# Kernel optimization log

Measured on AMD Instinct MI355X. Metric: run time of the kernel, lower is better.

## Reference

```python
import jax, jax.numpy as jnp
import numpy as np

N = 1024
IN_CH = 128
EDGE_CH = 32
OUT_CH = 128


def setup_inputs() -> dict:
    key = jax.random.key(0)
    ks = jax.random.split(key, 8)
    return {
        "node_mat": jax.random.normal(ks[0], (N, IN_CH), dtype=jnp.float32),
        "adj": jax.random.uniform(ks[1], (N, N), dtype=jnp.float32),
        "edge_adj": jax.random.uniform(ks[2], (EDGE_CH, N, N), dtype=jnp.float32),
        "node_weight": jax.random.normal(ks[3], (IN_CH, OUT_CH), dtype=jnp.float32) * 0.05,
        "edge_lay_1": jax.random.normal(ks[4], (EDGE_CH, OUT_CH - 1), dtype=jnp.float32) * 0.05,
        "edge_lay_2": jax.random.normal(ks[5], (OUT_CH - 1, OUT_CH), dtype=jnp.float32) * 0.05,
        "root": jax.random.normal(ks[6], (IN_CH, OUT_CH), dtype=jnp.float32) * 0.05,
        "bias": jax.random.normal(ks[7], (OUT_CH,), dtype=jnp.float32) * 0.05,
    }


def reference(node_mat, adj, edge_adj, node_weight, edge_lay_1, edge_lay_2, root, bias):
    # node message passing: adj-weighted sum of transformed node features  [N, out]
    sum_filter_node_msgs = adj @ (node_mat @ node_weight)
    # edge MLP: 2-layer with ReLU, applied over the edge-channel axis
    # edge_adj: [E, N, N]; edge_lay_1: [E, out-1] -> h1: [out-1, N, N]
    h1 = jnp.maximum(jnp.einsum('enm,eb->bnm', edge_adj, edge_lay_1), 0.0)
    # h1: [out-1, N, N]; edge_lay_2: [out-1, out] -> h2: [out, N, N]
    h2 = jnp.einsum('bnm,bo->onm', h1, edge_lay_2)
    # adjacency-weighted compression: e_compress[n, o] = sum_m h2[o, n, m] * adj[n, m]
    e_compress = jnp.einsum('onm,nm->no', h2, adj)
    root_info = node_mat @ root
    return sum_filter_node_msgs + e_compress + root_info + bias
```

## Files before the change

### kernel.cpp

```cpp
#include <hip/hip_runtime.h>
#include <hip/hip_bf16.h>

#define NN 1024
#define IN_CH 128
#define EDGE_CH 32
#define OUT_CH 128

typedef __attribute__((ext_vector_type(8))) short bf16x8;
typedef __attribute__((ext_vector_type(4))) float f32x4;

static __device__ __forceinline__ short f2bf(float f) {
    union { float f; unsigned u; } v; v.f = f;
    unsigned r = v.u + 0x7FFFu + ((v.u >> 16) & 1u);
    return (short)(r >> 16);
}

__global__ void node_gemm_kernel(const float* __restrict__ node_mat,
                                 const float* __restrict__ node_weight,
                                 const float* __restrict__ root,
                                 short* __restrict__ PT,
                                 float* __restrict__ R) {
    __shared__ float nm[2 * IN_CH];
    int tid = threadIdx.x;
    int n0 = blockIdx.x * 2;
    nm[tid] = node_mat[n0 * IN_CH + tid];
    __syncthreads();
    int o = tid & 127;
    int h = tid >> 7;
    const float* nr = &nm[h * IN_CH];
    float accp = 0.f, accr = 0.f;
#pragma unroll 8
    for (int c = 0; c < IN_CH; ++c) {
        float x = nr[c];
        accp += x * node_weight[c * OUT_CH + o];
        accr += x * root[c * OUT_CH + o];
    }
    R[(size_t)(n0 + h) * OUT_CH + o] = accr;
    PT[(size_t)o * NN + (n0 + h)] = f2bf(accp);
}

__global__ void edge_out_kernel(const float* __restrict__ edge_adj,
                                const float* __restrict__ adj,
                                const float* __restrict__ L1,
                                const float* __restrict__ L2,
                                const float* __restrict__ R,
                                const float* __restrict__ bias,
                                float* __restrict__ out) {
    int n = blockIdx.x;
    int tid = threadIdx.x;
    int wave = tid >> 6;
    int lane = tid & 63;
    int quad = lane >> 4;
    int col  = lane & 15;

    bf16x8 a_frag[8];
#pragma unroll
    for (int bt = 0; bt < 8; ++bt) {
        int b = bt * 16 + col;
#pragma unroll
        for (int j = 0; j < 8; ++j) {
            int e = quad * 8 + j;
            float v = (b < OUT_CH - 1) ? L1[e * (OUT_CH - 1) + b] : 0.0f;
            a_frag[bt][j] = f2bf(v);
        }
    }

    float g_acc[8][4];
#pragma unroll
    for (int bt = 0; bt < 8; ++bt)
#pragma unroll
        for (int r = 0; r < 4; ++r) g_acc[bt][r] = 0.0f;

    const float* adj_row = adj + (size_t)n * NN;
    const float* ea_base = edge_adj + (size_t)n * NN;

    for (int c = 0; c < 4; ++c) {
        int base = wave * 256 + c * 64;
        float adjv[4];
        bf16x8 bf[4];
#pragma unroll
        for (int s = 0; s < 4; ++s) {
            int m = base + s * 16 + col;
            adjv[s] = adj_row[m];
#pragma unroll
            for (int j = 0; j < 8; ++j) {
                size_t e = (size_t)(quad * 8 + j);
                bf[s][j] = f2bf(ea_base[e * (size_t)(NN * NN) + m]);
            }
        }
#pragma unroll
        for (int s = 0; s < 4; ++s) {
#pragma unroll
            for (int bt = 0; bt < 8; ++bt) {
                f32x4 d = __builtin_amdgcn_mfma_f32_16x16x32_bf16(
                    a_frag[bt], bf[s], (f32x4){0.f, 0.f, 0.f, 0.f}, 0, 0, 0);
#pragma unroll
                for (int r = 0; r < 4; ++r)
                    g_acc[bt][r] += fmaxf(d[r], 0.0f) * adjv[s];
            }
        }
    }

#pragma unroll
    for (int bt = 0; bt < 8; ++bt)
#pragma unroll
        for (int r = 0; r < 4; ++r) {
            float v = g_acc[bt][r];
            v += __shfl_xor(v, 1);
            v += __shfl_xor(v, 2);
            v += __shfl_xor(v, 4);
            v += __shfl_xor(v, 8);
            g_acc[bt][r] = v;
        }

    __shared__ float gred[4][OUT_CH];
    __shared__ float gs[OUT_CH];
    __shared__ float part[2][OUT_CH];
    if (col == 0) {
#pragma unroll
        for (int bt = 0; bt < 8; ++bt)
#pragma unroll
            for (int r = 0; r < 4; ++r)
                gred[wave][bt * 16 + quad * 4 + r] = g_acc[bt][r];
    }
    __syncthreads();
    if (tid < OUT_CH)
        gs[tid] = gred[0][tid] + gred[1][tid] + gred[2][tid] + gred[3][tid];
    __syncthreads();

    int o = tid & 127;
    int hf = tid >> 7;
    float acc = 0.f;
    int blo = hf * 64, bhi = hf ? 127 : 64;
#pragma unroll 8
    for (int b = blo; b < bhi; ++b)
        acc += gs[b] * L2[b * OUT_CH + o];
    part[hf][o] = acc;
    __syncthreads();
    if (tid < 128)
        out[(size_t)n * OUT_CH + tid] =
            part[0][tid] + part[1][tid] + R[(size_t)n * OUT_CH + tid] + bias[tid];
}

__global__ void adjp_kernel(const float* __restrict__ adj,
                            const short* __restrict__ PT,
                            float* __restrict__ out) {
    int blk = blockIdx.x;
    int nb = blk & 63;
    int oh = blk >> 6;
    int tid = threadIdx.x;
    int wave = tid >> 6;
    int lane = tid & 63;
    int quad = lane >> 4;
    int col  = lane & 15;
    int n0 = nb * 16;
    int o0 = oh * 64;

    f32x4 acc[4];
#pragma unroll
    for (int ot = 0; ot < 4; ++ot) acc[ot] = (f32x4){0.f, 0.f, 0.f, 0.f};

    int kbase = wave * 256;
#pragma unroll
    for (int ks = 0; ks < 8; ++ks) {
        int k = kbase + ks * 32 + quad * 8;
        const float* ap = adj + (size_t)(n0 + col) * NN + k;
        f32x4 a0 = *(const f32x4*)ap;
        f32x4 a1 = *(const f32x4*)(ap + 4);
        bf16x8 a;
#pragma unroll
        for (int j = 0; j < 4; ++j) { a[j] = f2bf(a0[j]); a[4 + j] = f2bf(a1[j]); }
#pragma unroll
        for (int ot = 0; ot < 4; ++ot) {
            int o = o0 + ot * 16 + col;
            bf16x8 b = *(const bf16x8*)(PT + (size_t)o * NN + k);
            acc[ot] = __builtin_amdgcn_mfma_f32_16x16x32_bf16(a, b, acc[ot], 0, 0, 0);
        }
    }

    __shared__ float red[4][16][65];
#pragma unroll
    for (int ot = 0; ot < 4; ++ot)
#pragma unroll
        for (int r = 0; r < 4; ++r)
            red[wave][quad * 4 + r][ot * 16 + col] = acc[ot][r];
    __syncthreads();

#pragma unroll
    for (int i = tid; i < 16 * 64; i += 256) {
        int rr = i >> 6;
        int cc = i & 63;
        float v = red[0][rr][cc] + red[1][rr][cc] + red[2][rr][cc] + red[3][rr][cc];
        out[(size_t)(n0 + rr) * OUT_CH + o0 + cc] += v;
    }
}

extern "C" void kernel_launch(void* const* d_in, const int* in_sizes, int n_in,
                              void* d_out, int out_size, void* d_ws, size_t ws_size,
                              hipStream_t stream) {
    const float* node_mat    = (const float*)d_in[0];
    const float* adj         = (const float*)d_in[1];
    const float* edge_adj    = (const float*)d_in[2];
    const float* node_weight = (const float*)d_in[3];
    const float* edge_lay_1  = (const float*)d_in[4];
    const float* edge_lay_2  = (const float*)d_in[5];
    const float* root        = (const float*)d_in[6];
    const float* bias        = (const float*)d_in[7];
    float* out = (float*)d_out;

    short* PT = (short*)d_ws;
    float* R  = (float*)((char*)d_ws + OUT_CH * NN * sizeof(short));

    node_gemm_kernel<<<NN / 2, 256, 0, stream>>>(node_mat, node_weight, root, PT, R);
    edge_out_kernel<<<NN, 256, 0, stream>>>(edge_adj, adj, edge_lay_1, edge_lay_2,
                                            R, bias, out);
    adjp_kernel<<<128, 256, 0, stream>>>(adj, PT, out);
}
```

Baseline: 243.9 us.

## Stage edge_adj through LDS with async global_load_lds double buffering

The edge kernel now loads edge_adj slices directly into a double-buffered LDS tile using global_load_lds 16-byte transfers, instead of scalar strided global loads. Each block rotates its chunk order by block index to spread DRAM access, and the compute for one chunk overlaps the prefetch of the next. Kernel order is swapped so adjp writes R and bias first and the edge kernel accumulates into out, and launch bounds are set for two blocks per CU. The cost is 64KB of LDS per block, which limits occupancy, plus an LDS read-and-convert step before each MFMA.

```diff
diff --git a/kernel.cpp b/kernel.cpp
--- a/kernel.cpp
+++ b/kernel.cpp
@@ -5,6 +5,7 @@
 #define IN_CH 128
 #define EDGE_CH 32
 #define OUT_CH 128
+#define NNSQ ((size_t)NN * (size_t)NN)
 
 typedef __attribute__((ext_vector_type(8))) short bf16x8;
 typedef __attribute__((ext_vector_type(4))) float f32x4;
@@ -39,111 +40,10 @@
     PT[(size_t)o * NN + (n0 + h)] = f2bf(accp);
 }
 
-__global__ void edge_out_kernel(const float* __restrict__ edge_adj,
-                                const float* __restrict__ adj,
-                                const float* __restrict__ L1,
-                                const float* __restrict__ L2,
-                                const float* __restrict__ R,
-                                const float* __restrict__ bias,
-                                float* __restrict__ out) {
-    int n = blockIdx.x;
-    int tid = threadIdx.x;
-    int wave = tid >> 6;
-    int lane = tid & 63;
-    int quad = lane >> 4;
-    int col  = lane & 15;
-
-    bf16x8 a_frag[8];
-#pragma unroll
-    for (int bt = 0; bt < 8; ++bt) {
-        int b = bt * 16 + col;
-#pragma unroll
-        for (int j = 0; j < 8; ++j) {
-            int e = quad * 8 + j;
-            float v = (b < OUT_CH - 1) ? L1[e * (OUT_CH - 1) + b] : 0.0f;
-            a_frag[bt][j] = f2bf(v);
-        }
-    }
-
-    float g_acc[8][4];
-#pragma unroll
-    for (int bt = 0; bt < 8; ++bt)
-#pragma unroll
-        for (int r = 0; r < 4; ++r) g_acc[bt][r] = 0.0f;
-
-    const float* adj_row = adj + (size_t)n * NN;
-    const float* ea_base = edge_adj + (size_t)n * NN;
-
-    for (int c = 0; c < 4; ++c) {
-        int base = wave * 256 + c * 64;
-        float adjv[4];
-        bf16x8 bf[4];
-#pragma unroll
-        for (int s = 0; s < 4; ++s) {
-            int m = base + s * 16 + col;
-            adjv[s] = adj_row[m];
-#pragma unroll
-            for (int j = 0; j < 8; ++j) {
-                size_t e = (size_t)(quad * 8 + j);
-                bf[s][j] = f2bf(ea_base[e * (size_t)(NN * NN) + m]);
-            }
-        }
-#pragma unroll
-        for (int s = 0; s < 4; ++s) {
-#pragma unroll
-            for (int bt = 0; bt < 8; ++bt) {
-                f32x4 d = __builtin_amdgcn_mfma_f32_16x16x32_bf16(
-                    a_frag[bt], bf[s], (f32x4){0.f, 0.f, 0.f, 0.f}, 0, 0, 0);
-#pragma unroll
-                for (int r = 0; r < 4; ++r)
-                    g_acc[bt][r] += fmaxf(d[r], 0.0f) * adjv[s];
-            }
-        }
-    }
-
-#pragma unroll
-    for (int bt = 0; bt < 8; ++bt)
-#pragma unroll
-        for (int r = 0; r < 4; ++r) {
-            float v = g_acc[bt][r];
-            v += __shfl_xor(v, 1);
-            v += __shfl_xor(v, 2);
-            v += __shfl_xor(v, 4);
-            v += __shfl_xor(v, 8);
-            g_acc[bt][r] = v;
-        }
-
-    __shared__ float gred[4][OUT_CH];
-    __shared__ float gs[OUT_CH];
-    __shared__ float part[2][OUT_CH];
-    if (col == 0) {
-#pragma unroll
-        for (int bt = 0; bt < 8; ++bt)
-#pragma unroll
-            for (int r = 0; r < 4; ++r)
-                gred[wave][bt * 16 + quad * 4 + r] = g_acc[bt][r];
-    }
-    __syncthreads();
-    if (tid < OUT_CH)
-        gs[tid] = gred[0][tid] + gred[1][tid] + gred[2][tid] + gred[3][tid];
-    __syncthreads();
-
-    int o = tid & 127;
-    int hf = tid >> 7;
-    float acc = 0.f;
-    int blo = hf * 64, bhi = hf ? 127 : 64;
-#pragma unroll 8
-    for (int b = blo; b < bhi; ++b)
-        acc += gs[b] * L2[b * OUT_CH + o];
-    part[hf][o] = acc;
-    __syncthreads();
-    if (tid < 128)
-        out[(size_t)n * OUT_CH + tid] =
-            part[0][tid] + part[1][tid] + R[(size_t)n * OUT_CH + tid] + bias[tid];
-}
-
 __global__ void adjp_kernel(const float* __restrict__ adj,
                             const short* __restrict__ PT,
+                            const float* __restrict__ R,
+                            const float* __restrict__ bias,
                             float* __restrict__ out) {
     int blk = blockIdx.x;
     int nb = blk & 63;
@@ -191,7 +91,136 @@
         int rr = i >> 6;
         int cc = i & 63;
         float v = red[0][rr][cc] + red[1][rr][cc] + red[2][rr][cc] + red[3][rr][cc];
-        out[(size_t)(n0 + rr) * OUT_CH + o0 + cc] += v;
+        size_t idx = (size_t)(n0 + rr) * OUT_CH + o0 + cc;
+        out[idx] = v + R[idx] + bias[o0 + cc];
+    }
+}
+
+__global__ void __launch_bounds__(256, 2)
+edge_out_kernel(const float* __restrict__ edge_adj,
+                const float* __restrict__ adj,
+                const float* __restrict__ L1,
+                const float* __restrict__ L2,
+                float* __restrict__ out) {
+    int n = blockIdx.x;
+    int tid = threadIdx.x;
+    int wave = tid >> 6;
+    int lane = tid & 63;
+    int quad = lane >> 4;
+    int col  = lane & 15;
+
+    __shared__ __attribute__((aligned(16))) float ea_lds[2][32 * 256];
+
+    bf16x8 a_frag[8];
+#pragma unroll
+    for (int bt = 0; bt < 8; ++bt) {
+        int b = bt * 16 + col;
+#pragma unroll
+        for (int j = 0; j < 8; ++j) {
+            int e = quad * 8 + j;
+            float v = (b < OUT_CH - 1) ? L1[e * (OUT_CH - 1) + b] : 0.0f;
+            a_frag[bt][j] = f2bf(v);
+        }
+    }
+
+    float g_acc[8][4];
+#pragma unroll
+    for (int bt = 0; bt < 8; ++bt)
+#pragma unroll
+        for (int r = 0; r < 4; ++r) g_acc[bt][r] = 0.0f;
+
+    const int cr0 = n & 3, cr1 = (n + 1) & 3, cr2 = (n + 2) & 3, cr3 = (n + 3) & 3;
+    float adjv[4][4];
+    {
+        const float* ar = adj + (size_t)n * NN + wave * 64 + col;
+#pragma unroll
+        for (int s = 0; s < 4; ++s) {
+            adjv[0][s] = ar[cr0 * 256 + s * 16];
+            adjv[1][s] = ar[cr1 * 256 + s * 16];
+            adjv[2][s] = ar[cr2 * 256 + s * 16];
+            adjv[3][s] = ar[cr3 * 256 + s * 16];
+        }
+    }
+
+    int rot = wave * 8;
+    int moff = (lane * 4 + rot) & 255;
+    const float* ea_base = edge_adj + (size_t)(wave * 8) * NNSQ + (size_t)n * NN + moff;
+
+#define STAGE(BUFIDX, AC) { \
+        const float* g_ = ea_base + (AC) * 256; \
+        float* l_ = &ea_lds[BUFIDX][wave * 8 * 256]; \
+        _Pragma("unroll") for (int j = 0; j < 8; ++j) { \
+            __builtin_amdgcn_global_load_lds( \
+                (const __attribute__((address_space(1))) unsigned*)(g_ + j * NNSQ), \
+                (__attribute__((address_space(3))) unsigned*)(l_ + j * 256), \
+                16, 0, 0); } }
+#define COMPUTE(BUFIDX, CI) { \
+        _Pragma("unroll") for (int s = 0; s < 4; ++s) { \
+            int mloc = wave * 64 + s * 16 + col; \
+            int d = (mloc - quad * 8) & 255;          \
+            const float* bp = &ea_lds[BUFIDX][quad * 8 * 256 + d]; \
+            bf16x8 bfv; \
+            _Pragma("unroll") for (int j = 0; j < 8; ++j) \
+                bfv[j] = f2bf(bp[j * 256]); \
+            float av = adjv[CI][s]; \
+            _Pragma("unroll") for (int bt = 0; bt < 8; ++bt) { \
+                f32x4 dd = __builtin_amdgcn_mfma_f32_16x16x32_bf16( \
+                    a_frag[bt], bfv, (f32x4){0.f, 0.f, 0.f, 0.f}, 0, 0, 0); \
+                _Pragma("unroll") for (int r = 0; r < 4; ++r) \
+                    g_acc[bt][r] += fmaxf(dd[r], 0.0f) * av; } } }
+
+    STAGE(0, cr0);
+    __syncthreads();
+    STAGE(1, cr1); COMPUTE(0, 0); __syncthreads();
+    STAGE(0, cr2); COMPUTE(1, 1); __syncthreads();
+    STAGE(1, cr3); COMPUTE(0, 2); __syncthreads();
+    COMPUTE(1, 3);
+    __syncthreads();
+
+#undef STAGE
+#undef COMPUTE
+
+#pragma unroll
+    for (int bt = 0; bt < 8; ++bt)
+#pragma unroll
+        for (int r = 0; r < 4; ++r) {
+            float v = g_acc[bt][r];
+            v += __shfl_xor(v, 1);
+            v += __shfl_xor(v, 2);
+            v += __shfl_xor(v, 4);
+            v += __shfl_xor(v, 8);
+            g_acc[bt][r] = v;
+        }
+
+    float* gred = &ea_lds[0][0];
+    float* gs   = gred + 4 * OUT_CH;
+    float* part = gs + OUT_CH;
+
+    if (col == 0) {
+#pragma unroll
+        for (int bt = 0; bt < 8; ++bt)
+#pragma unroll
+            for (int r = 0; r < 4; ++r)
+                gred[wave * OUT_CH + bt * 16 + quad * 4 + r] = g_acc[bt][r];
+    }
+    __syncthreads();
+    if (tid < OUT_CH)
+        gs[tid] = gred[0 * OUT_CH + tid] + gred[1 * OUT_CH + tid] +
+                  gred[2 * OUT_CH + tid] + gred[3 * OUT_CH + tid];
+    __syncthreads();
+
+    int o = tid & 127;
+    int hf = tid >> 7;
+    float acc = 0.f;
+    int blo = hf * 64, bhi = hf ? 127 : 64;
+#pragma unroll 8
+    for (int b = blo; b < bhi; ++b)
+        acc += gs[b] * L2[b * OUT_CH + o];
+    part[hf * OUT_CH + o] = acc;
+    __syncthreads();
+    if (tid < 128) {
+        size_t idx = (size_t)n * OUT_CH + tid;
+        out[idx] += part[0 * OUT_CH + tid] + part[1 * OUT_CH + tid];
     }
 }
 
@@ -212,7 +241,7 @@
     float* R  = (float*)((char*)d_ws + OUT_CH * NN * sizeof(short));
 
     node_gemm_kernel<<<NN / 2, 256, 0, stream>>>(node_mat, node_weight, root, PT, R);
-    edge_out_kernel<<<NN, 256, 0, stream>>>(edge_adj, adj, edge_lay_1, edge_lay_2,
-                                            R, bias, out);
-    adjp_kernel<<<128, 256, 0, stream>>>(adj, PT, out);
-}
+    adjp_kernel<<<128, 256, 0, stream>>>(adj, PT, R, bias, out);
+    edge_out_kernel<<<NN, 256, 0, stream>>>(edge_adj, adj, edge_lay_1,
+                                            edge_lay_2, out);
+}
```

New measurement: 284.6 us. 16.7% more time.
